# Kernel tuning notes

Measured on AMD Instinct MI355X. Metric: run time of the kernel, lower is better.

Reference implementation:

```python
import jax, jax.numpy as jnp
import numpy as np

N, E, B, NPG, LD, LT = 32768, 524288, 256, 128, 100, 1000

def conv1d(x, w, b):
    # x: [B, Cin, L], w: [Cout, Cin, K]
    y = jax.lax.conv_general_dilated(x, w, (1,), 'VALID', dimension_numbers=('NCH', 'OIH', 'NCH'))
    return y + b[None, :, None]

def conv_branch(x, w1, b1, w2, b2, w3, b3):
    x = jax.nn.relu(conv1d(x, w1, b1))
    x = jax.nn.relu(conv1d(x, w2, b2))
    x = jax.nn.relu(conv1d(x, w3, b3))
    return x.max(axis=2)  # global max pool over length

def gat(x, src, dst, ea, W, a_s, a_d, We, a_e, bias, heads, ch):
    # PyG GATConv with edge_dim, add_self_loops=True (fill_value='mean'), concat=True
    n = x.shape[0]
    loop = jnp.arange(n)
    src = jnp.concatenate([src, loop])
    dst = jnp.concatenate([dst, loop])
    ea = jnp.concatenate([ea, jnp.broadcast_to(ea.mean(0), (n, ea.shape[1]))], 0)
    h = (x @ W).reshape(n, heads, ch)                               # [N,H,C]
    a = (h * a_s).sum(-1)[src] + (h * a_d).sum(-1)[dst] \
        + ((ea @ We).reshape(-1, heads, ch) * a_e).sum(-1)          # [E+N,H]
    a = jax.nn.leaky_relu(a, 0.2)
    amax = jax.ops.segment_max(a, dst, num_segments=n)
    ex = jnp.exp(a - amax[dst])
    alpha = ex / (jax.ops.segment_sum(ex, dst, num_segments=n)[dst] + 1e-16)
    out = jax.ops.segment_sum(h[src] * alpha[..., None], dst, num_segments=n)
    return out.reshape(n, heads * ch) + bias

def reference(xd, xt, ax, ei, ea, batch, emb_xd, emb_xt, wd1, bd1, wd2, bd2, wd3, bd3, wt1, bt1, wt2, bt2, wt3, bt3, g1_w, g1_as, g1_ad, g1_we, g1_ae, g1_b, g2_w, g2_as, g2_ad, g2_we, g2_ae, g2_b, fc1_w, fc1_b, c1_w, c1_b, c2_w, c2_b, c3_w, c3_b, c4_w, c4_b):
    cd = conv_branch(emb_xd[xd].transpose(0, 2, 1), wd1, bd1, wd2, bd2, wd3, bd3)  # [B,96]
    ct = conv_branch(emb_xt[xt].transpose(0, 2, 1), wt1, bt1, wt2, bt2, wt3, bt3)  # [B,96]
    src, dst = ei[0], ei[1]
    g = jax.nn.elu(gat(ax, src, dst, ea, g1_w, g1_as, g1_ad, g1_we, g1_ae, g1_b, 5, 64))
    g = jax.nn.relu(gat(g, src, dst, ea, g2_w, g2_as, g2_ad, g2_we, g2_ae, g2_b, 1, 96))
    g = jax.ops.segment_max(g, batch, num_segments=B)               # global max pool per graph
    g = jax.nn.relu(g @ fc1_w + fc1_b)
    xc = jnp.concatenate([cd, ct, g], axis=1)                        # [B,288]
    h = jax.nn.relu(xc @ c1_w + c1_b)
    h = jax.nn.relu(h @ c2_w + c2_b)
    h = jax.nn.relu(h @ c3_w + c3_b)
    return h @ c4_w + c4_b                                           # [B,1]

def setup_inputs():
    ks = iter(jax.random.split(jax.random.key(0), 64))
    def nrm(*shape):
        return jax.random.normal(next(ks), shape, jnp.float32) * 0.05
    d = {}
    d['xd'] = jax.random.randint(next(ks), (B, LD), 0, 65, jnp.int32)
    d['xt'] = jax.random.randint(next(ks), (B, LT), 0, 26, jnp.int32)
    d['ax'] = jax.random.normal(next(ks), (N, 24), jnp.float32)
    gid = jax.random.randint(next(ks), (E,), 0, B)
    so = jax.random.randint(next(ks), (E,), 0, NPG)
    do = jax.random.randint(next(ks), (E,), 0, NPG)
    d['ei'] = jnp.stack([gid * NPG + so, gid * NPG + do]).astype(jnp.int32)
    d['ea'] = jax.random.normal(next(ks), (E, 5), jnp.float32)
    d['batch'] = jnp.repeat(jnp.arange(B, dtype=jnp.int32), NPG)
    d['emb_xd'] = nrm(65, 128); d['emb_xt'] = nrm(26, 128)
    d['wd1'] = nrm(32, 128, 4); d['bd1'] = nrm(32)
    d['wd2'] = nrm(64, 32, 4); d['bd2'] = nrm(64)
    d['wd3'] = nrm(96, 64, 4); d['bd3'] = nrm(96)
    d['wt1'] = nrm(32, 128, 8); d['bt1'] = nrm(32)
    d['wt2'] = nrm(64, 32, 8); d['bt2'] = nrm(64)
    d['wt3'] = nrm(96, 64, 8); d['bt3'] = nrm(96)
    d['g1_w'] = nrm(24, 320); d['g1_as'] = nrm(5, 64); d['g1_ad'] = nrm(5, 64)
    d['g1_we'] = nrm(5, 320); d['g1_ae'] = nrm(5, 64); d['g1_b'] = nrm(320)
    d['g2_w'] = nrm(320, 96); d['g2_as'] = nrm(1, 96); d['g2_ad'] = nrm(1, 96)
    d['g2_we'] = nrm(5, 96); d['g2_ae'] = nrm(1, 96); d['g2_b'] = nrm(96)
    d['fc1_w'] = nrm(96, 96); d['fc1_b'] = nrm(96)
    d['c1_w'] = nrm(288, 1024); d['c1_b'] = nrm(1024)
    d['c2_w'] = nrm(1024, 1024); d['c2_b'] = nrm(1024)
    d['c3_w'] = nrm(1024, 512); d['c3_b'] = nrm(512)
    d['c4_w'] = nrm(512, 1); d['c4_b'] = nrm(1)
    return d
```

## Files before the change

kernel.cpp:

```cpp
#include <hip/hip_runtime.h>

constexpr int NN = 32768;
constexpr int EE = 524288;
constexpr int NB = 256;
constexpr int EN = EE + NN;

typedef unsigned short u16;
typedef short bh8 __attribute__((ext_vector_type(8)));
typedef float f32x4 __attribute__((ext_vector_type(4)));

__device__ inline u16 f2b(float f) {
  unsigned u = __float_as_uint(f);
  return (u16)((u + 0x7fffu + ((u >> 16) & 1u)) >> 16);
}

constexpr size_t MB = 1ull << 20;
constexpr size_t OFF_A    = 0;
constexpr size_t OFF_B    = 48*MB;
constexpr size_t OFF_AC   = 100*MB;
constexpr size_t OFF_C    = 116*MB;
constexpr size_t OFF_CSRS = 130*MB;
constexpr size_t OFF_CSRE = 133*MB;
constexpr size_t OFF_ROWP = 136*MB;
constexpr size_t OFF_DEG  = 137*MB;
constexpr size_t OFF_CUR  = 138*MB;
constexpr size_t OFF_A2   = 139*MB;
constexpr size_t OFF_G2O  = 142*MB;
constexpr size_t OFF_AS1  = 155*MB;
constexpr size_t OFF_AD1  = 156*MB;
constexpr size_t OFF_AS2  = 157*MB;
constexpr size_t OFF_AD2  = 158*MB;
constexpr size_t OFF_CD   = 159*MB;
constexpr size_t OFF_CT   = 160*MB;
constexpr size_t OFF_POOL = 161*MB;
constexpr size_t OFF_GFC  = 162*MB;
constexpr size_t OFF_XC   = 163*MB;
constexpr size_t OFF_M1B  = 164*MB;
constexpr size_t OFF_M2B  = 165*MB;
constexpr size_t OFF_M3B  = 166*MB;
constexpr size_t OFF_FD   = 167*MB;
constexpr size_t OFF_FT   = 168*MB;
constexpr size_t OFF_WD2T = 169*MB;
constexpr size_t OFF_WD3T = 170*MB;
constexpr size_t OFF_WT2B = 171*MB;
constexpr size_t OFF_WT3B = 172*MB;
constexpr size_t OFF_W2GB = 174*MB;
constexpr size_t OFF_CB   = 173*MB;

__global__ void k_tables(const float* __restrict__ wd1, const float* __restrict__ emb_xd,
                         const float* __restrict__ wt1, const float* __restrict__ emb_xt,
                         const float* __restrict__ g1we, const float* __restrict__ g1ae,
                         const float* __restrict__ g2we, const float* __restrict__ g2ae,
                         float* __restrict__ Fd, float* __restrict__ Ft,
                         float* __restrict__ CB) {
  int t = blockIdx.x * 256 + threadIdx.x;
  const int NFd = 32*4*65, NFt = 32*8*26;
  if (t < NFd) {
    int v = t % 65; int ck = t / 65; int k = ck & 3; int co = ck >> 2;
    float s = 0.f;
    for (int ci = 0; ci < 128; ++ci)
      s = fmaf(wd1[(co*128 + ci)*4 + k], emb_xd[v*128 + ci], s);
    Fd[t] = s;
  } else if (t < NFd + NFt) {
    int u = t - NFd;
    int v = u % 26; int ck = u / 26; int k = ck & 7; int co = ck >> 3;
    float s = 0.f;
    for (int ci = 0; ci < 128; ++ci)
      s = fmaf(wt1[(co*128 + ci)*8 + k], emb_xt[v*128 + ci], s);
    Ft[(k*26 + v)*32 + co] = s;
  } else if (t < NFd + NFt + 25) {
    int u = t - NFd - NFt; int h = u % 5, j = u / 5;
    float s = 0.f;
    for (int c = 0; c < 64; ++c)
      s = fmaf(g1we[j*320 + h*64 + c], g1ae[h*64 + c], s);
    CB[j*5 + h] = s;
  } else if (t < NFd + NFt + 30) {
    int j = t - NFd - NFt - 25;
    float s = 0.f;
    for (int c = 0; c < 96; ++c)
      s = fmaf(g2we[j*96 + c], g2ae[c], s);
    CB[25 + j] = s;
  }
}

__global__ void k_wcvt(const float* __restrict__ w2, const float* __restrict__ w3,
                       const float* __restrict__ g2w,
                       u16* __restrict__ o2, u16* __restrict__ o3,
                       u16* __restrict__ og2) {
  int t = blockIdx.x*256 + threadIdx.x;
  if (t < 64*256) {
    int co = t >> 8, k = t & 255, kk = k >> 5, ci = k & 31;
    o2[t] = f2b(w2[(co*32 + ci)*8 + kk]);
  } else if (t < 64*256 + 96*512) {
    int u = t - 64*256;
    int co = u >> 9, k = u & 511, kk = k >> 6, ci = k & 63;
    o3[u] = f2b(w3[(co*64 + ci)*8 + kk]);
  } else if (t < 64*256 + 96*512 + 96*320) {
    int u = t - 64*256 - 96*512;
    int co = u / 320, k = u % 320;
    og2[u] = f2b(g2w[k*96 + co]);
  }
}

__global__ void k_easum(const float* __restrict__ ea, float* __restrict__ CB) {
  float acc[5] = {0,0,0,0,0};
  for (long e = blockIdx.x*256L + threadIdx.x; e < EE; e += 256L*gridDim.x) {
    #pragma unroll
    for (int j = 0; j < 5; ++j) acc[j] += ea[e*5 + j];
  }
  #pragma unroll
  for (int j = 0; j < 5; ++j)
    for (int off = 1; off < 64; off <<= 1) acc[j] += __shfl_xor(acc[j], off, 64);
  if ((threadIdx.x & 63) == 0) {
    #pragma unroll
    for (int j = 0; j < 5; ++j) atomicAdd(&CB[30 + j], acc[j]);
  }
}

__global__ void k_finalize(float* __restrict__ CB) {
  if (blockIdx.x == 0 && threadIdx.x == 0) {
    float em[5];
    for (int j = 0; j < 5; ++j) { em[j] = CB[30 + j] / (float)EE; CB[41 + j] = em[j]; }
    for (int h = 0; h < 5; ++h) {
      float s = 0.f;
      for (int j = 0; j < 5; ++j) s = fmaf(em[j], CB[j*5 + h], s);
      CB[35 + h] = s;
    }
    float s = 0.f;
    for (int j = 0; j < 5; ++j) s = fmaf(em[j], CB[25 + j], s);
    CB[40] = s;
  }
}

template<int K, int V, int COUT>
__global__ void k_conv1_lut(const int* __restrict__ idx, const float* __restrict__ F,
                            const float* __restrict__ bias, float* __restrict__ y,
                            int L, int Lout) {
  __shared__ float Fs[COUT*K*V];
  __shared__ float bs[COUT];
  int b = blockIdx.y;
  for (int i = threadIdx.x; i < COUT*K*V; i += blockDim.x) Fs[i] = F[i];
  for (int i = threadIdx.x; i < COUT; i += blockDim.x) bs[i] = bias[i];
  __syncthreads();
  int o = blockIdx.x * blockDim.x + threadIdx.x;
  if (o >= COUT * Lout) return;
  int co = o / Lout, l = o % Lout;
  const int* ib = idx + b*L + l;
  float acc = bs[co];
  #pragma unroll
  for (int k = 0; k < K; ++k) acc += Fs[(co*K + k)*V + ib[k]];
  y[(b*COUT + co)*Lout + l] = fmaxf(acc, 0.f);
}

__global__ __launch_bounds__(512) void k_conv1t(
    const int* __restrict__ idx, const float* __restrict__ Ftab,
    const float* __restrict__ bias, u16* __restrict__ y, int L, int Lout) {
  constexpr int K = 8, V = 26, CO = 32;
  __shared__ float Fs[K*V*CO];
  __shared__ float bs[CO];
  __shared__ int sq[16 + K];
  int b = blockIdx.y, l0 = blockIdx.x * 16;
  for (int i = threadIdx.x; i < K*V*CO; i += 512) Fs[i] = Ftab[i];
  if (threadIdx.x < CO) bs[threadIdx.x] = bias[threadIdx.x];
  if (threadIdx.x < 16 + K - 1) {
    int l = l0 + (int)threadIdx.x;
    sq[threadIdx.x] = (l < L) ? idx[b*L + l] : 0;
  }
  __syncthreads();
  int co = threadIdx.x & 31;
  int p = threadIdx.x >> 5;
  int l = l0 + p;
  if (l >= Lout) return;
  float acc = bs[co];
  #pragma unroll
  for (int k = 0; k < K; ++k) acc += Fs[(k*V + sq[p + k])*CO + co];
  y[((size_t)b*Lout + l)*CO + co] = f2b(fmaxf(acc, 0.f));
}

__global__ void k_wtrans(const float* __restrict__ w, float* __restrict__ wt,
                         int COUT, int CIN, int K) {
  int t = blockIdx.x*256 + threadIdx.x;
  if (t >= COUT*CIN*K) return;
  int k = t % K; int ci = (t / K) % CIN; int co = t / (K*CIN);
  wt[(ci*K + k)*COUT + co] = w[t];
}

template<int CIN, int K, int COUT, int G, int LG, bool POOL>
__global__ void k_conv(const float* __restrict__ x, const float* __restrict__ wt,
                       const float* __restrict__ bias, float* __restrict__ y,
                       int Lin, int Lout) {
  constexpr int LT = G * LG;
  __shared__ float xs[CIN][LT + K - 1];
  int b = blockIdx.y;
  int l0 = blockIdx.x * LT;
  const int nth = COUT * G;
  const float* xb = x + b*CIN*Lin;
  for (int i = threadIdx.x; i < CIN*(LT + K - 1); i += nth) {
    int ci = i / (LT + K - 1), dl = i % (LT + K - 1);
    int l = l0 + dl;
    xs[ci][dl] = (l < Lin) ? xb[ci*Lin + l] : 0.f;
  }
  __syncthreads();
  int co = threadIdx.x % COUT;
  int gg = threadIdx.x / COUT;
  float acc[LG];
  #pragma unroll
  for (int j = 0; j < LG; ++j) acc[j] = 0.f;
  for (int ci = 0; ci < CIN; ++ci) {
    float xr[LG + K - 1];
    #pragma unroll
    for (int t = 0; t < LG + K - 1; ++t) xr[t] = xs[ci][gg*LG + t];
    #pragma unroll
    for (int k = 0; k < K; ++k) {
      float wv = wt[(ci*K + k)*COUT + co];
      #pragma unroll
      for (int j = 0; j < LG; ++j) acc[j] = fmaf(wv, xr[j + k], acc[j]);
    }
  }
  float bv = bias[co];
  if (!POOL) {
    float* yb = y + (b*COUT + co)*Lout;
    #pragma unroll
    for (int j = 0; j < LG; ++j) {
      int l = l0 + gg*LG + j;
      if (l < Lout) yb[l] = fmaxf(acc[j] + bv, 0.f);
    }
  } else {
    float m = 0.f;
    #pragma unroll
    for (int j = 0; j < LG; ++j) {
      int l = l0 + gg*LG + j;
      if (l < Lout) m = fmaxf(m, fmaxf(acc[j] + bv, 0.f));
    }
    atomicMax((unsigned int*)&y[b*COUT + co], __float_as_uint(m));
  }
}

template<int CIN, int COUT, int NT2, bool POOL>
__global__ __launch_bounds__(512) void k_convmfma(
    const u16* __restrict__ xin, const u16* __restrict__ wtb,
    const float* __restrict__ bias, u16* __restrict__ yout,
    unsigned int* __restrict__ pool, int Lin, int Lout) {
  constexpr int KD = CIN*8;
  constexpr int NCH = KD/32;
  constexpr int MT = 256, ROWS = MT + 7;
  constexpr int XPAD = CIN + 8;
  constexpr int WPAD = KD + 8;
  __shared__ u16 xs[ROWS*XPAD];
  __shared__ u16 wsd[COUT*WPAD];
  int b = blockIdx.y;
  int l0 = blockIdx.x * MT;
  int tid = threadIdx.x;
  {
    const unsigned* wg = (const unsigned*)wtb;
    unsigned* wl = (unsigned*)wsd;
    constexpr int KD2 = KD/2, WP2 = WPAD/2;
    for (int i = tid; i < COUT*KD2; i += 512) {
      int co = i / KD2, c = i % KD2;
      wl[co*WP2 + c] = wg[i];
    }
  }
  {
    const unsigned* xg = (const unsigned*)(xin + (size_t)b*Lin*CIN);
    unsigned* xl = (unsigned*)xs;
    constexpr int C2 = CIN/2, XP2 = XPAD/2;
    for (int i = tid; i < ROWS*C2; i += 512) {
      int r = i / C2, c = i % C2;
      unsigned v = 0;
      if (l0 + r < Lin) v = xg[(size_t)l0*C2 + i];
      xl[r*XP2 + c] = v;
    }
  }
  __syncthreads();
  int lane = tid & 63;
  int w = tid >> 6;
  int mg = w & 3, ng = w >> 2;
  int l15 = lane & 15, l4 = lane >> 4;
  f32x4 acc[4][NT2];
  #pragma unroll
  for (int mi = 0; mi < 4; ++mi)
    #pragma unroll
    for (int nj = 0; nj < NT2; ++nj) acc[mi][nj] = (f32x4){0.f, 0.f, 0.f, 0.f};

  #pragma unroll
  for (int ch = 0; ch < NCH; ++ch) {
    const int kk = (ch*32) / CIN;
    const int cib = (ch*32) % CIN + l4*8;
    bh8 a[4], bb[NT2];
    #pragma unroll
    for (int mi = 0; mi < 4; ++mi) {
      int row = mg*64 + mi*16 + l15 + kk;
      a[mi] = *(const bh8*)&xs[row*XPAD + cib];
    }
    #pragma unroll
    for (int nj = 0; nj < NT2; ++nj) {
      int co = (ng*NT2 + nj)*16 + l15;
      bb[nj] = *(const bh8*)&wsd[co*WPAD + ch*32 + l4*8];
    }
    #pragma unroll
    for (int mi = 0; mi < 4; ++mi)
      #pragma unroll
      for (int nj = 0; nj < NT2; ++nj)
        acc[mi][nj] = __builtin_amdgcn_mfma_f32_16x16x32_bf16(a[mi], bb[nj], acc[mi][nj], 0, 0, 0);
  }

  if (!POOL) {
    #pragma unroll
    for (int nj = 0; nj < NT2; ++nj) {
      int co = (ng*NT2 + nj)*16 + l15;
      float bv = bias[co];
      #pragma unroll
      for (int mi = 0; mi < 4; ++mi)
        #pragma unroll
        for (int r = 0; r < 4; ++r) {
          int m = mg*64 + mi*16 + l4*4 + r;
          if (l0 + m < Lout)
            yout[((size_t)b*Lout + l0 + m)*COUT + co] = f2b(fmaxf(acc[mi][nj][r] + bv, 0.f));
        }
    }
  } else {
    #pragma unroll
    for (int nj = 0; nj < NT2; ++nj) {
      int co = (ng*NT2 + nj)*16 + l15;
      float bv = bias[co];
      float mx = 0.f;
      #pragma unroll
      for (int mi = 0; mi < 4; ++mi)
        #pragma unroll
        for (int r = 0; r < 4; ++r) {
          int m = mg*64 + mi*16 + l4*4 + r;
          if (l0 + m < Lout) mx = fmaxf(mx, fmaxf(acc[mi][nj][r] + bv, 0.f));
        }
      mx = fmaxf(mx, __shfl_xor(mx, 16, 64));
      mx = fmaxf(mx, __shfl_xor(mx, 32, 64));
      if (l4 == 0) atomicMax(&pool[b*COUT + co], __float_as_uint(mx));
    }
  }
}

__global__ __launch_bounds__(512) void k_h2mfma(
    const u16* __restrict__ g1ob, const u16* __restrict__ wb,
    float* __restrict__ h2) {
  constexpr int KD = 320, WPAD = 328, NCH = 10;
  __shared__ u16 wsd[96*WPAD];
  int tid = threadIdx.x;
  {
    const unsigned* wg = (const unsigned*)wb;
    unsigned* wl = (unsigned*)wsd;
    for (int i = tid; i < 96*(KD/2); i += 512) {
      int co = i / (KD/2), c = i % (KD/2);
      wl[co*(WPAD/2) + c] = wg[i];
    }
  }
  __syncthreads();
  int lane = tid & 63;
  int w = tid >> 6;
  int l15 = lane & 15, l4 = lane >> 4;
  long m0 = (long)blockIdx.x * 128;
  const u16* xr = g1ob + (m0 + w*16 + l15) * KD;
  f32x4 acc[6];
  #pragma unroll
  for (int nj = 0; nj < 6; ++nj) acc[nj] = (f32x4){0.f, 0.f, 0.f, 0.f};
  #pragma unroll
  for (int ch = 0; ch < NCH; ++ch) {
    bh8 a = *(const bh8*)&xr[ch*32 + l4*8];
    #pragma unroll
    for (int nj = 0; nj < 6; ++nj) {
      bh8 b = *(const bh8*)&wsd[(nj*16 + l15)*WPAD + ch*32 + l4*8];
      acc[nj] = __builtin_amdgcn_mfma_f32_16x16x32_bf16(a, b, acc[nj], 0, 0, 0);
    }
  }
  #pragma unroll
  for (int nj = 0; nj < 6; ++nj) {
    #pragma unroll
    for (int r = 0; r < 4; ++r) {
      long row = m0 + w*16 + l4*4 + r;
      h2[row*96 + nj*16 + l15] = acc[nj][r];
    }
  }
}

template<int BM, int BN, int BK, int TM, int TN, bool BIAS, bool RELU>
__global__ void k_gemm(const float* __restrict__ X, const float* __restrict__ W,
                       const float* __restrict__ bias, float* __restrict__ Y,
                       int K, int C) {
  constexpr int NTH = (BM/TM)*(BN/TN);
  static_assert(NTH == 256, "block must be 256 threads");
  __shared__ float xs[BK][BM + 1];
  __shared__ float wsm[BK][BN];
  const int m0 = blockIdx.y * BM;
  const int c0 = blockIdx.x * BN;
  const int tn = threadIdx.x % (BN/TN);
  const int tm = threadIdx.x / (BN/TN);
  float acc[TM][TN];
  #pragma unroll
  for (int i = 0; i < TM; ++i)
    #pragma unroll
    for (int j = 0; j < TN; ++j) acc[i][j] = 0.f;

  for (int k0 = 0; k0 < K; k0 += BK) {
    #pragma unroll
    for (int i = threadIdx.x; i < BM*BK; i += NTH) {
      int m = i / BK, k = i % BK;
      xs[k][m] = X[(long)(m0 + m)*K + k0 + k];
    }
    #pragma unroll
    for (int i = threadIdx.x; i < BK*BN; i += NTH) {
      int k = i / BN, c = i % BN;
      wsm[k][c] = W[(long)(k0 + k)*C + c0 + c];
    }
    __syncthreads();
    #pragma unroll
    for (int k = 0; k < BK; ++k) {
      float xv[TM], wv[TN];
      #pragma unroll
      for (int i = 0; i < TM; ++i) xv[i] = xs[k][tm*TM + i];
      #pragma unroll
      for (int j = 0; j < TN; ++j) wv[j] = wsm[k][tn*TN + j];
      #pragma unroll
      for (int i = 0; i < TM; ++i)
        #pragma unroll
        for (int j = 0; j < TN; ++j) acc[i][j] = fmaf(xv[i], wv[j], acc[i][j]);
    }
    __syncthreads();
  }
  #pragma unroll
  for (int i = 0; i < TM; ++i) {
    float* yr = Y + (long)(m0 + tm*TM + i)*C + c0 + tn*TN;
    #pragma unroll
    for (int j = 0; j < TN; ++j) {
      float v = acc[i][j];
      if (BIAS) v += bias[c0 + tn*TN + j];
      if (RELU) v = fmaxf(v, 0.f);
      yr[j] = v;
    }
  }
}

template<int BM, int BN, int BK, int TM, int TN>
__global__ void k_gemm_sk(const float* __restrict__ X, const float* __restrict__ W,
                          float* __restrict__ Y, int K, int C, int KS) {
  constexpr int NTH = (BM/TM)*(BN/TN);
  static_assert(NTH == 256, "block must be 256 threads");
  __shared__ float xs[BK][BM + 1];
  __shared__ float wsm[BK][BN];
  const int m0 = blockIdx.y * BM;
  const int c0 = blockIdx.x * BN;
  const int kbeg = blockIdx.z * KS;
  const int kend = min(K, kbeg + KS);
  const int tn = threadIdx.x % (BN/TN);
  const int tm = threadIdx.x / (BN/TN);
  float acc[TM][TN];
  #pragma unroll
  for (int i = 0; i < TM; ++i)
    #pragma unroll
    for (int j = 0; j < TN; ++j) acc[i][j] = 0.f;

  for (int k0 = kbeg; k0 < kend; k0 += BK) {
    #pragma unroll
    for (int i = threadIdx.x; i < BM*BK; i += NTH) {
      int m = i / BK, k = i % BK;
      xs[k][m] = X[(long)(m0 + m)*K + k0 + k];
    }
    #pragma unroll
    for (int i = threadIdx.x; i < BK*BN; i += NTH) {
      int k = i / BN, c = i % BN;
      wsm[k][c] = W[(long)(k0 + k)*C + c0 + c];
    }
    __syncthreads();
    #pragma unroll
    for (int k = 0; k < BK; ++k) {
      float xv[TM], wv[TN];
      #pragma unroll
      for (int i = 0; i < TM; ++i) xv[i] = xs[k][tm*TM + i];
      #pragma unroll
      for (int j = 0; j < TN; ++j) wv[j] = wsm[k][tn*TN + j];
      #pragma unroll
      for (int i = 0; i < TM; ++i)
        #pragma unroll
        for (int j = 0; j < TN; ++j) acc[i][j] = fmaf(xv[i], wv[j], acc[i][j]);
    }
    __syncthreads();
  }
  #pragma unroll
  for (int i = 0; i < TM; ++i) {
    float* yr = Y + (long)(m0 + tm*TM + i)*C + c0 + tn*TN;
    #pragma unroll
    for (int j = 0; j < TN; ++j) atomicAdd(&yr[j], acc[i][j]);
  }
}

__global__ void k_bias_relu(float* __restrict__ Y, const float* __restrict__ bias,
                            long total, int C, int relu) {
  long o = blockIdx.x*256L + threadIdx.x;
  if (o >= total) return;
  int c = (int)(o % C);
  float v = Y[o] + bias[c];
  if (relu) v = fmaxf(v, 0.f);
  Y[o] = v;
}

__global__ void k_attn_nodeterms(const float* __restrict__ h, const float* __restrict__ a_s,
                                 const float* __restrict__ a_d, float* __restrict__ as_o,
                                 float* __restrict__ ad_o, int H, int CH) {
  long t = blockIdx.x*256L + threadIdx.x;
  if (t >= (long)NN * H) return;
  int n = (int)(t / H), hh = (int)(t % H);
  const float* hr = h + ((long)n*H + hh)*CH;
  float s1 = 0.f, s2 = 0.f;
  for (int c = 0; c < CH; ++c) {
    float v = hr[c];
    s1 = fmaf(v, a_s[hh*CH + c], s1);
    s2 = fmaf(v, a_d[hh*CH + c], s2);
  }
  as_o[t] = s1; ad_o[t] = s2;
}

template<int H>
__global__ void k_edge_attn(const int* __restrict__ ei, const float* __restrict__ ea,
                            const float* __restrict__ asb, const float* __restrict__ adb,
                            const float* __restrict__ M, const float* __restrict__ aeself,
                            float* __restrict__ a_out) {
  long e = blockIdx.x*256L + threadIdx.x;
  if (e >= (long)EN) return;
  int s, d;
  float av[H];
  if (e < EE) {
    s = ei[e]; d = ei[EE + e];
    float er[5];
    #pragma unroll
    for (int j = 0; j < 5; ++j) er[j] = ea[e*5 + j];
    #pragma unroll
    for (int h = 0; h < H; ++h) {
      float t = 0.f;
      #pragma unroll
      for (int j = 0; j < 5; ++j) t = fmaf(er[j], M[j*H + h], t);
      av[h] = t;
    }
  } else {
    s = d = (int)(e - EE);
    #pragma unroll
    for (int h = 0; h < H; ++h) av[h] = aeself[h];
  }
  #pragma unroll
  for (int h = 0; h < H; ++h) {
    float v = asb[s*H + h] + adb[d*H + h] + av[h];
    a_out[e*H + h] = (v > 0.f) ? v : 0.2f * v;
  }
}

template<int H>
__global__ void k_acsr(const int* __restrict__ csr_eid, const float* __restrict__ a,
                       float* __restrict__ ac) {
  long p = blockIdx.x*256L + threadIdx.x;
  if (p >= (long)EN) return;
  long e = csr_eid[p];
  #pragma unroll
  for (int h = 0; h < H; ++h) ac[p*H + h] = a[e*H + h];
}

__global__ void k_deg(const int* __restrict__ ei, int* __restrict__ deg) {
  long e = blockIdx.x*256L + threadIdx.x;
  if (e >= (long)EN) return;
  int d = (e < EE) ? ei[EE + e] : (int)(e - EE);
  atomicAdd(&deg[d], 1);
}

__global__ void k_scan(const int* __restrict__ deg, int* __restrict__ rowptr,
                       int* __restrict__ cursor) {
  __shared__ int ps[256];
  int tid = threadIdx.x;
  int base = tid * 128;
  int s = 0;
  for (int i = 0; i < 128; ++i) s += deg[base + i];
  ps[tid] = s;
  __syncthreads();
  for (int off = 1; off < 256; off <<= 1) {
    int v = (tid >= off) ? ps[tid - off] : 0;
    __syncthreads();
    ps[tid] += v;
    __syncthreads();
  }
  int run = ps[tid] - s;
  for (int i = 0; i < 128; ++i) {
    rowptr[base + i] = run;
    cursor[base + i] = run;
    run += deg[base + i];
  }
  if (tid == 255) rowptr[NN] = run;
}

__global__ void k_scatter(const int* __restrict__ ei, int* __restrict__ cursor,
                          int* __restrict__ csr_src, int* __restrict__ csr_eid) {
  long e = blockIdx.x*256L + threadIdx.x;
  if (e >= (long)EN) return;
  int s, d;
  if (e < EE) { s = ei[e]; d = ei[EE + e]; }
  else        { s = d = (int)(e - EE); }
  int p = atomicAdd(&cursor[d], 1);
  csr_src[p] = s;
  csr_eid[p] = (int)e;
}

template<int H, int CH, int ACT, bool OBF16>
__global__ void k_gat_aggr(const int* __restrict__ rowptr, const int* __restrict__ csr_src,
                           const float* __restrict__ ac,
                           const float* __restrict__ hfeat, const float* __restrict__ bias,
                           void* __restrict__ outv) {
  int bid = blockIdx.x;
  int x = bid & 7;
  int r = bid >> 3;
  int s = r & 31;
  int c = r >> 5;
  int g = c*8 + x;
  int wid = g*128 + s*4 + (int)(threadIdx.x >> 6);
  int lane = threadIdx.x & 63;
  int row0 = rowptr[wid], row1 = rowptr[wid + 1];
  constexpr int F = H * CH;
  constexpr int NJ = (F + 63) / 64;
  float amax[H], asum[H], rinv[H];
  #pragma unroll
  for (int h = 0; h < H; ++h) amax[h] = -1e30f;
  for (int p = row0 + lane; p < row1; p += 64) {
    #pragma unroll
    for (int h = 0; h < H; ++h) amax[h] = fmaxf(amax[h], ac[(long)p*H + h]);
  }
  #pragma unroll
  for (int h = 0; h < H; ++h)
    for (int off = 1; off < 64; off <<= 1) amax[h] = fmaxf(amax[h], __shfl_xor(amax[h], off, 64));
  #pragma unroll
  for (int h = 0; h < H; ++h) asum[h] = 0.f;
  for (int p = row0 + lane; p < row1; p += 64) {
    #pragma unroll
    for (int h = 0; h < H; ++h) asum[h] += __expf(ac[(long)p*H + h] - amax[h]);
  }
  #pragma unroll
  for (int h = 0; h < H; ++h) {
    for (int off = 1; off < 64; off <<= 1) asum[h] += __shfl_xor(asum[h], off, 64);
    rinv[h] = 1.f / (asum[h] + 1e-16f);
  }
  float acc[NJ];
  #pragma unroll
  for (int j = 0; j < NJ; ++j) acc[j] = 0.f;
  for (int p = row0; p < row1; ++p) {
    int src = csr_src[p];
    const float* hr = hfeat + (long)src * F;
    #pragma unroll
    for (int j = 0; j < NJ; ++j) {
      int idx = j*64 + lane;
      if ((F % 64 == 0) || idx < F) {
        int h = idx / CH;
        float al = __expf(ac[(long)p*H + h] - amax[h]) * rinv[h];
        acc[j] = fmaf(al, hr[idx], acc[j]);
      }
    }
  }
  #pragma unroll
  for (int j = 0; j < NJ; ++j) {
    int idx = j*64 + lane;
    if ((F % 64 == 0) || idx < F) {
      float v = acc[j] + bias[idx];
      if (ACT == 0) v = (v > 0.f) ? v : expm1f(v);
      else          v = fmaxf(v, 0.f);
      if (OBF16) ((u16*)outv)[(long)wid * F + idx] = f2b(v);
      else       ((float*)outv)[(long)wid * F + idx] = v;
    }
  }
}

__global__ void k_pool(const float* __restrict__ g2o, const int* __restrict__ batch,
                       unsigned int* __restrict__ pooled) {
  long o = blockIdx.x*256L + threadIdx.x;
  if (o >= (long)NN * 96) return;
  int n = (int)(o / 96), c = (int)(o % 96);
  atomicMax(&pooled[batch[n]*96 + c], __float_as_uint(g2o[o]));
}

__global__ void k_concat(const float* __restrict__ cd, const float* __restrict__ ct,
                         const float* __restrict__ gfc, float* __restrict__ xc) {
  int t = blockIdx.x*256 + threadIdx.x;
  if (t >= NB*288) return;
  int b = t / 288, c = t % 288;
  float v = (c < 96) ? cd[b*96 + c] : (c < 192) ? ct[b*96 + (c-96)] : gfc[b*96 + (c-192)];
  xc[t] = v;
}

__global__ void k_final(const float* __restrict__ x, const float* __restrict__ w,
                        const float* __restrict__ b, float* __restrict__ out) {
  int wid = (int)((blockIdx.x*256L + threadIdx.x) >> 6);
  int lane = threadIdx.x & 63;
  if (wid >= NB) return;
  const float* xr = x + (long)wid*512;
  float s = 0.f;
  for (int k = lane; k < 512; k += 64) s = fmaf(xr[k], w[k], s);
  for (int off = 1; off < 64; off <<= 1) s += __shfl_xor(s, off, 64);
  if (lane == 0) out[wid] = s + b[0];
}

extern "C" void kernel_launch(void* const* d_in, const int* in_sizes, int n_in,
                              void* d_out, int out_size, void* d_ws, size_t ws_size,
                              hipStream_t stream) {
  const int*   xd     = (const int*)  d_in[0];
  const int*   xt     = (const int*)  d_in[1];
  const float* ax     = (const float*)d_in[2];
  const int*   ei     = (const int*)  d_in[3];
  const float* ea     = (const float*)d_in[4];
  const int*   batch  = (const int*)  d_in[5];
  const float* emb_xd = (const float*)d_in[6];
  const float* emb_xt = (const float*)d_in[7];
  const float* wd1 = (const float*)d_in[8];  const float* bd1 = (const float*)d_in[9];
  const float* wd2 = (const float*)d_in[10]; const float* bd2 = (const float*)d_in[11];
  const float* wd3 = (const float*)d_in[12]; const float* bd3 = (const float*)d_in[13];
  const float* wt1 = (const float*)d_in[14]; const float* bt1 = (const float*)d_in[15];
  const float* wt2 = (const float*)d_in[16]; const float* bt2 = (const float*)d_in[17];
  const float* wt3 = (const float*)d_in[18]; const float* bt3 = (const float*)d_in[19];
  const float* g1_w  = (const float*)d_in[20]; const float* g1_as = (const float*)d_in[21];
  const float* g1_ad = (const float*)d_in[22]; const float* g1_we = (const float*)d_in[23];
  const float* g1_ae = (const float*)d_in[24]; const float* g1_b  = (const float*)d_in[25];
  const float* g2_w  = (const float*)d_in[26]; const float* g2_as = (const float*)d_in[27];
  const float* g2_ad = (const float*)d_in[28]; const float* g2_we = (const float*)d_in[29];
  const float* g2_ae = (const float*)d_in[30]; const float* g2_b  = (const float*)d_in[31];
  const float* fc1_w = (const float*)d_in[32]; const float* fc1_b = (const float*)d_in[33];
  const float* c1_w = (const float*)d_in[34]; const float* c1_b = (const float*)d_in[35];
  const float* c2_w = (const float*)d_in[36]; const float* c2_b = (const float*)d_in[37];
  const float* c3_w = (const float*)d_in[38]; const float* c3_b = (const float*)d_in[39];
  const float* c4_w = (const float*)d_in[40]; const float* c4_b = (const float*)d_in[41];
  float* out = (float*)d_out;

  char* ws = (char*)d_ws;
  auto F = [&](size_t off) { return (float*)(ws + off); };
  auto I = [&](size_t off) { return (int*)(ws + off); };
  auto U = [&](size_t off) { return (unsigned int*)(ws + off); };
  auto H = [&](size_t off) { return (u16*)(ws + off); };

  hipMemsetAsync(ws + OFF_CB,   0, 64*sizeof(float), stream);
  hipMemsetAsync(ws + OFF_DEG,  0, NN*sizeof(int),   stream);
  hipMemsetAsync(ws + OFF_CD,   0, NB*96*sizeof(float), stream);
  hipMemsetAsync(ws + OFF_CT,   0, NB*96*sizeof(float), stream);
  hipMemsetAsync(ws + OFF_POOL, 0, NB*96*sizeof(float), stream);
  hipMemsetAsync(ws + OFF_GFC,  0, NB*96*sizeof(float),   stream);
  hipMemsetAsync(ws + OFF_M1B,  0, NB*1024*sizeof(float), stream);
  hipMemsetAsync(ws + OFF_M2B,  0, NB*1024*sizeof(float), stream);
  hipMemsetAsync(ws + OFF_M3B,  0, NB*512*sizeof(float),  stream);

  k_tables<<<(8320 + 6656 + 30 + 255)/256, 256, 0, stream>>>(
      wd1, emb_xd, wt1, emb_xt, g1_we, g1_ae, g2_we, g2_ae,
      F(OFF_FD), F(OFF_FT), F(OFF_CB));
  k_wcvt<<<(64*256 + 96*512 + 96*320 + 255)/256, 256, 0, stream>>>(
      wt2, wt3, g2_w, H(OFF_WT2B), H(OFF_WT3B), H(OFF_W2GB));
  k_easum<<<256, 256, 0, stream>>>(ea, F(OFF_CB));
  k_finalize<<<1, 64, 0, stream>>>(F(OFF_CB));

  k_wtrans<<<(8192 + 255)/256, 256, 0, stream>>>(wd2, F(OFF_WD2T), 64, 32, 4);
  k_wtrans<<<(24576 + 255)/256, 256, 0, stream>>>(wd3, F(OFF_WD3T), 96, 64, 4);

  k_conv1_lut<4,65,32><<<dim3((32*97 + 255)/256, NB), 256, 0, stream>>>(
      xd, F(OFF_FD), bd1, F(OFF_A), 100, 97);
  k_conv<32,4,64,4,16,false><<<dim3((94 + 63)/64, NB), 256, 0, stream>>>(
      F(OFF_A), F(OFF_WD2T), bd2, F(OFF_B), 97, 94);
  k_conv<64,4,96,2,16,true><<<dim3((91 + 31)/32, NB), 192, 0, stream>>>(
      F(OFF_B), F(OFF_WD3T), bd3, F(OFF_CD), 94, 91);

  k_conv1t<<<dim3((993 + 15)/16, NB), 512, 0, stream>>>(
      xt, F(OFF_FT), bt1, H(OFF_A), 1000, 993);
  k_convmfma<32,64,2,false><<<dim3(4, NB), 512, 0, stream>>>(
      H(OFF_A), H(OFF_WT2B), bt2, H(OFF_B), nullptr, 993, 986);
  k_convmfma<64,96,3,true><<<dim3(4, NB), 512, 0, stream>>>(
      H(OFF_B), H(OFF_WT3B), bt3, nullptr, U(OFF_CT), 986, 979);

  k_deg<<<(EN + 255)/256, 256, 0, stream>>>(ei, I(OFF_DEG));
  k_scan<<<1, 256, 0, stream>>>(I(OFF_DEG), I(OFF_ROWP), I(OFF_CUR));
  k_scatter<<<(EN + 255)/256, 256, 0, stream>>>(ei, I(OFF_CUR), I(OFF_CSRS), I(OFF_CSRE));

  k_gemm<64,64,24,4,4,false,false><<<dim3(320/64, NN/64), 256, 0, stream>>>(
      ax, g1_w, nullptr, F(OFF_A), 24, 320);
  k_attn_nodeterms<<<(NN*5 + 255)/256, 256, 0, stream>>>(
      F(OFF_A), g1_as, g1_ad, F(OFF_AS1), F(OFF_AD1), 5, 64);
  k_edge_attn<5><<<(EN + 255)/256, 256, 0, stream>>>(
      ei, ea, F(OFF_AS1), F(OFF_AD1), F(OFF_CB), F(OFF_CB) + 35, F(OFF_C));
  k_acsr<5><<<(EN + 255)/256, 256, 0, stream>>>(
      I(OFF_CSRE), F(OFF_C), F(OFF_AC));
  k_gat_aggr<5,64,0,true><<<NN/4, 256, 0, stream>>>(
      I(OFF_ROWP), I(OFF_CSRS), F(OFF_AC), F(OFF_A), g1_b, (void*)H(OFF_B));

  k_h2mfma<<<NN/128, 512, 0, stream>>>(H(OFF_B), H(OFF_W2GB), F(OFF_C));
  k_attn_nodeterms<<<(NN + 255)/256, 256, 0, stream>>>(
      F(OFF_C), g2_as, g2_ad, F(OFF_AS2), F(OFF_AD2), 1, 96);
  k_edge_attn<1><<<(EN + 255)/256, 256, 0, stream>>>(
      ei, ea, F(OFF_AS2), F(OFF_AD2), F(OFF_CB) + 25, F(OFF_CB) + 40, F(OFF_A2));
  k_acsr<1><<<(EN + 255)/256, 256, 0, stream>>>(
      I(OFF_CSRE), F(OFF_A2), F(OFF_AC));
  k_gat_aggr<1,96,1,false><<<NN/4, 256, 0, stream>>>(
      I(OFF_ROWP), I(OFF_CSRS), F(OFF_AC), F(OFF_C), g2_b, (void*)F(OFF_G2O));

  k_pool<<<(int)(((long)NN*96 + 255)/256), 256, 0, stream>>>(
      F(OFF_G2O), batch, U(OFF_POOL));
  k_gemm_sk<64,32,32,4,2><<<dim3(96/32, NB/64, 3), 256, 0, stream>>>(
      F(OFF_POOL), fc1_w, F(OFF_GFC), 96, 96, 32);
  k_bias_relu<<<(NB*96 + 255)/256, 256, 0, stream>>>(
      F(OFF_GFC), fc1_b, (long)NB*96, 96, 1);

  k_concat<<<(NB*288 + 255)/256, 256, 0, stream>>>(
      F(OFF_CD), F(OFF_CT), F(OFF_GFC), F(OFF_XC));

  k_gemm_sk<64,64,32,4,4><<<dim3(1024/64, NB/64, 3), 256, 0, stream>>>(
      F(OFF_XC), c1_w, F(OFF_M1B), 288, 1024, 96);
  k_bias_relu<<<(NB*1024 + 255)/256, 256, 0, stream>>>(
      F(OFF_M1B), c1_b, (long)NB*1024, 1024, 1);

  k_gemm_sk<64,64,32,4,4><<<dim3(1024/64, NB/64, 8), 256, 0, stream>>>(
      F(OFF_M1B), c2_w, F(OFF_M2B), 1024, 1024, 128);
  k_bias_relu<<<(NB*1024 + 255)/256, 256, 0, stream>>>(
      F(OFF_M2B), c2_b, (long)NB*1024, 1024, 1);

  k_gemm_sk<64,64,32,4,4><<<dim3(512/64, NB/64, 8), 256, 0, stream>>>(
      F(OFF_M2B), c3_w, F(OFF_M3B), 1024, 512, 128);
  k_bias_relu<<<(NB*512 + 255)/256, 256, 0, stream>>>(
      F(OFF_M3B), c3_b, (long)NB*512, 512, 1);

  k_final<<<(NB*64 + 255)/256, 256, 0, stream>>>(F(OFF_M3B), c4_w, c4_b, out);
}
```

Measured before the change: 882.4 us.

## Move drug conv branch to bf16 MFMA and split GAT softmax into separate kernels

The drug-sequence conv branch now uses the same LUT-based first layer and bf16 MFMA conv kernels as the target branch, replacing the fp32 scalar conv kernels and the weight transpose kernels. Separately, the GAT softmax max/sum pass moves out of the aggregation kernel into a per-node stats kernel, followed by an edge-parallel kernel that writes normalized alpha in place. For that, the CSR build now also records each edge's destination. The aggregation kernel then only does the weighted sum, at the cost of two extra launches per layer and extra passes over the edge array.

```diff
diff --git a/kernel.cpp b/kernel.cpp
--- a/kernel.cpp
+++ b/kernel.cpp
@@ -18,6 +18,7 @@
 constexpr size_t OFF_A    = 0;
 constexpr size_t OFF_B    = 48*MB;
 constexpr size_t OFF_AC   = 100*MB;
+constexpr size_t OFF_CSRD = 112*MB;
 constexpr size_t OFF_C    = 116*MB;
 constexpr size_t OFF_CSRS = 130*MB;
 constexpr size_t OFF_CSRE = 133*MB;
@@ -40,8 +41,8 @@
 constexpr size_t OFF_M3B  = 166*MB;
 constexpr size_t OFF_FD   = 167*MB;
 constexpr size_t OFF_FT   = 168*MB;
-constexpr size_t OFF_WD2T = 169*MB;
-constexpr size_t OFF_WD3T = 170*MB;
+constexpr size_t OFF_WD2B = 169*MB;
+constexpr size_t OFF_WD3B = 170*MB;
 constexpr size_t OFF_WT2B = 171*MB;
 constexpr size_t OFF_WT3B = 172*MB;
 constexpr size_t OFF_W2GB = 174*MB;
@@ -60,7 +61,7 @@
     float s = 0.f;
     for (int ci = 0; ci < 128; ++ci)
       s = fmaf(wd1[(co*128 + ci)*4 + k], emb_xd[v*128 + ci], s);
-    Fd[t] = s;
+    Fd[(k*65 + v)*32 + co] = s;
   } else if (t < NFd + NFt) {
     int u = t - NFd;
     int v = u % 26; int ck = u / 26; int k = ck & 7; int co = ck >> 3;
@@ -83,22 +84,28 @@
   }
 }
 
-__global__ void k_wcvt(const float* __restrict__ w2, const float* __restrict__ w3,
+__global__ void k_wcvt(const float* __restrict__ wd2, const float* __restrict__ wd3,
+                       const float* __restrict__ wt2, const float* __restrict__ wt3,
                        const float* __restrict__ g2w,
-                       u16* __restrict__ o2, u16* __restrict__ o3,
+                       u16* __restrict__ od2, u16* __restrict__ od3,
+                       u16* __restrict__ ot2, u16* __restrict__ ot3,
                        u16* __restrict__ og2) {
   int t = blockIdx.x*256 + threadIdx.x;
-  if (t < 64*256) {
+  if (t < 8192) {
+    int co = t >> 7, k = t & 127, kk = k >> 5, ci = k & 31;
+    od2[t] = f2b(wd2[(co*32 + ci)*4 + kk]);
+  } else if ((t -= 8192) < 24576) {
+    int co = t >> 8, k = t & 255, kk = k >> 6, ci = k & 63;
+    od3[t] = f2b(wd3[(co*64 + ci)*4 + kk]);
+  } else if ((t -= 24576) < 16384) {
     int co = t >> 8, k = t & 255, kk = k >> 5, ci = k & 31;
-    o2[t] = f2b(w2[(co*32 + ci)*8 + kk]);
-  } else if (t < 64*256 + 96*512) {
-    int u = t - 64*256;
-    int co = u >> 9, k = u & 511, kk = k >> 6, ci = k & 63;
-    o3[u] = f2b(w3[(co*64 + ci)*8 + kk]);
-  } else if (t < 64*256 + 96*512 + 96*320) {
-    int u = t - 64*256 - 96*512;
-    int co = u / 320, k = u % 320;
-    og2[u] = f2b(g2w[k*96 + co]);
+    ot2[t] = f2b(wt2[(co*32 + ci)*8 + kk]);
+  } else if ((t -= 16384) < 49152) {
+    int co = t >> 9, k = t & 511, kk = k >> 6, ci = k & 63;
+    ot3[t] = f2b(wt3[(co*64 + ci)*8 + kk]);
+  } else if ((t -= 49152) < 30720) {
+    int co = t / 320, k = t % 320;
+    og2[t] = f2b(g2w[k*96 + co]);
   }
 }
 
@@ -132,30 +139,11 @@
   }
 }
 
-template<int K, int V, int COUT>
-__global__ void k_conv1_lut(const int* __restrict__ idx, const float* __restrict__ F,
-                            const float* __restrict__ bias, float* __restrict__ y,
-                            int L, int Lout) {
-  __shared__ float Fs[COUT*K*V];
-  __shared__ float bs[COUT];
-  int b = blockIdx.y;
-  for (int i = threadIdx.x; i < COUT*K*V; i += blockDim.x) Fs[i] = F[i];
-  for (int i = threadIdx.x; i < COUT; i += blockDim.x) bs[i] = bias[i];
-  __syncthreads();
-  int o = blockIdx.x * blockDim.x + threadIdx.x;
-  if (o >= COUT * Lout) return;
-  int co = o / Lout, l = o % Lout;
-  const int* ib = idx + b*L + l;
-  float acc = bs[co];
-  #pragma unroll
-  for (int k = 0; k < K; ++k) acc += Fs[(co*K + k)*V + ib[k]];
-  y[(b*COUT + co)*Lout + l] = fmaxf(acc, 0.f);
-}
-
+template<int K, int V>
 __global__ __launch_bounds__(512) void k_conv1t(
     const int* __restrict__ idx, const float* __restrict__ Ftab,
     const float* __restrict__ bias, u16* __restrict__ y, int L, int Lout) {
-  constexpr int K = 8, V = 26, CO = 32;
+  constexpr int CO = 32;
   __shared__ float Fs[K*V*CO];
   __shared__ float bs[CO];
   __shared__ int sq[16 + K];
@@ -177,73 +165,14 @@
   y[((size_t)b*Lout + l)*CO + co] = f2b(fmaxf(acc, 0.f));
 }
 
-__global__ void k_wtrans(const float* __restrict__ w, float* __restrict__ wt,
-                         int COUT, int CIN, int K) {
-  int t = blockIdx.x*256 + threadIdx.x;
-  if (t >= COUT*CIN*K) return;
-  int k = t % K; int ci = (t / K) % CIN; int co = t / (K*CIN);
-  wt[(ci*K + k)*COUT + co] = w[t];
-}
-
-template<int CIN, int K, int COUT, int G, int LG, bool POOL>
-__global__ void k_conv(const float* __restrict__ x, const float* __restrict__ wt,
-                       const float* __restrict__ bias, float* __restrict__ y,
-                       int Lin, int Lout) {
-  constexpr int LT = G * LG;
-  __shared__ float xs[CIN][LT + K - 1];
-  int b = blockIdx.y;
-  int l0 = blockIdx.x * LT;
-  const int nth = COUT * G;
-  const float* xb = x + b*CIN*Lin;
-  for (int i = threadIdx.x; i < CIN*(LT + K - 1); i += nth) {
-    int ci = i / (LT + K - 1), dl = i % (LT + K - 1);
-    int l = l0 + dl;
-    xs[ci][dl] = (l < Lin) ? xb[ci*Lin + l] : 0.f;
-  }
-  __syncthreads();
-  int co = threadIdx.x % COUT;
-  int gg = threadIdx.x / COUT;
-  float acc[LG];
-  #pragma unroll
-  for (int j = 0; j < LG; ++j) acc[j] = 0.f;
-  for (int ci = 0; ci < CIN; ++ci) {
-    float xr[LG + K - 1];
-    #pragma unroll
-    for (int t = 0; t < LG + K - 1; ++t) xr[t] = xs[ci][gg*LG + t];
-    #pragma unroll
-    for (int k = 0; k < K; ++k) {
-      float wv = wt[(ci*K + k)*COUT + co];
-      #pragma unroll
-      for (int j = 0; j < LG; ++j) acc[j] = fmaf(wv, xr[j + k], acc[j]);
-    }
-  }
-  float bv = bias[co];
-  if (!POOL) {
-    float* yb = y + (b*COUT + co)*Lout;
-    #pragma unroll
-    for (int j = 0; j < LG; ++j) {
-      int l = l0 + gg*LG + j;
-      if (l < Lout) yb[l] = fmaxf(acc[j] + bv, 0.f);
-    }
-  } else {
-    float m = 0.f;
-    #pragma unroll
-    for (int j = 0; j < LG; ++j) {
-      int l = l0 + gg*LG + j;
-      if (l < Lout) m = fmaxf(m, fmaxf(acc[j] + bv, 0.f));
-    }
-    atomicMax((unsigned int*)&y[b*COUT + co], __float_as_uint(m));
-  }
-}
-
-template<int CIN, int COUT, int NT2, bool POOL>
+template<int CIN, int KK, int COUT, int NT2, bool POOL>
 __global__ __launch_bounds__(512) void k_convmfma(
     const u16* __restrict__ xin, const u16* __restrict__ wtb,
     const float* __restrict__ bias, u16* __restrict__ yout,
     unsigned int* __restrict__ pool, int Lin, int Lout) {
-  constexpr int KD = CIN*8;
+  constexpr int KD = CIN*KK;
   constexpr int NCH = KD/32;
-  constexpr int MT = 256, ROWS = MT + 7;
+  constexpr int MT = 256, ROWS = MT + KK - 1;
   constexpr int XPAD = CIN + 8;
   constexpr int WPAD = KD + 8;
   __shared__ u16 xs[ROWS*XPAD];
@@ -559,6 +488,52 @@
   for (int h = 0; h < H; ++h) ac[p*H + h] = a[e*H + h];
 }
 
+template<int H>
+__global__ void k_stats(const int* __restrict__ rowptr, const float* __restrict__ ac,
+                        float* __restrict__ amaxo, float* __restrict__ rinvo) {
+  int wid = (int)((blockIdx.x*256L + threadIdx.x) >> 6);
+  int lane = threadIdx.x & 63;
+  if (wid >= NN) return;
+  int row0 = rowptr[wid], row1 = rowptr[wid + 1];
+  float amax[H], asum[H];
+  #pragma unroll
+  for (int h = 0; h < H; ++h) amax[h] = -1e30f;
+  for (int p = row0 + lane; p < row1; p += 64) {
+    #pragma unroll
+    for (int h = 0; h < H; ++h) amax[h] = fmaxf(amax[h], ac[(long)p*H + h]);
+  }
+  #pragma unroll
+  for (int h = 0; h < H; ++h)
+    for (int off = 1; off < 64; off <<= 1) amax[h] = fmaxf(amax[h], __shfl_xor(amax[h], off, 64));
+  #pragma unroll
+  for (int h = 0; h < H; ++h) asum[h] = 0.f;
+  for (int p = row0 + lane; p < row1; p += 64) {
+    #pragma unroll
+    for (int h = 0; h < H; ++h) asum[h] += __expf(ac[(long)p*H + h] - amax[h]);
+  }
+  #pragma unroll
+  for (int h = 0; h < H; ++h)
+    for (int off = 1; off < 64; off <<= 1) asum[h] += __shfl_xor(asum[h], off, 64);
+  if (lane == 0) {
+    #pragma unroll
+    for (int h = 0; h < H; ++h) {
+      amaxo[(long)wid*H + h] = amax[h];
+      rinvo[(long)wid*H + h] = 1.f / (asum[h] + 1e-16f);
+    }
+  }
+}
+
+template<int H>
+__global__ void k_alpha(const int* __restrict__ csr_dst, const float* __restrict__ amaxb,
+                        const float* __restrict__ rinvb, float* __restrict__ ac) {
+  long p = blockIdx.x*256L + threadIdx.x;
+  if (p >= (long)EN) return;
+  int d = csr_dst[p];
+  #pragma unroll
+  for (int h = 0; h < H; ++h)
+    ac[p*H + h] = __expf(ac[p*H + h] - amaxb[(long)d*H + h]) * rinvb[(long)d*H + h];
+}
+
 __global__ void k_deg(const int* __restrict__ ei, int* __restrict__ deg) {
   long e = blockIdx.x*256L + threadIdx.x;
   if (e >= (long)EN) return;
@@ -591,7 +566,8 @@
 }
 
 __global__ void k_scatter(const int* __restrict__ ei, int* __restrict__ cursor,
-                          int* __restrict__ csr_src, int* __restrict__ csr_eid) {
+                          int* __restrict__ csr_src, int* __restrict__ csr_eid,
+                          int* __restrict__ csr_dst) {
   long e = blockIdx.x*256L + threadIdx.x;
   if (e >= (long)EN) return;
   int s, d;
@@ -600,6 +576,7 @@
   int p = atomicAdd(&cursor[d], 1);
   csr_src[p] = s;
   csr_eid[p] = (int)e;
+  csr_dst[p] = d;
 }
 
 template<int H, int CH, int ACT, bool OBF16>
@@ -618,27 +595,6 @@
   int row0 = rowptr[wid], row1 = rowptr[wid + 1];
   constexpr int F = H * CH;
   constexpr int NJ = (F + 63) / 64;
-  float amax[H], asum[H], rinv[H];
-  #pragma unroll
-  for (int h = 0; h < H; ++h) amax[h] = -1e30f;
-  for (int p = row0 + lane; p < row1; p += 64) {
-    #pragma unroll
-    for (int h = 0; h < H; ++h) amax[h] = fmaxf(amax[h], ac[(long)p*H + h]);
-  }
-  #pragma unroll
-  for (int h = 0; h < H; ++h)
-    for (int off = 1; off < 64; off <<= 1) amax[h] = fmaxf(amax[h], __shfl_xor(amax[h], off, 64));
-  #pragma unroll
-  for (int h = 0; h < H; ++h) asum[h] = 0.f;
-  for (int p = row0 + lane; p < row1; p += 64) {
-    #pragma unroll
-    for (int h = 0; h < H; ++h) asum[h] += __expf(ac[(long)p*H + h] - amax[h]);
-  }
-  #pragma unroll
-  for (int h = 0; h < H; ++h) {
-    for (int off = 1; off < 64; off <<= 1) asum[h] += __shfl_xor(asum[h], off, 64);
-    rinv[h] = 1.f / (asum[h] + 1e-16f);
-  }
   float acc[NJ];
   #pragma unroll
   for (int j = 0; j < NJ; ++j) acc[j] = 0.f;
@@ -650,8 +606,7 @@
       int idx = j*64 + lane;
       if ((F % 64 == 0) || idx < F) {
         int h = idx / CH;
-        float al = __expf(ac[(long)p*H + h] - amax[h]) * rinv[h];
-        acc[j] = fmaf(al, hr[idx], acc[j]);
+        acc[j] = fmaf(ac[(long)p*H + h], hr[idx], acc[j]);
       }
     }
   }
@@ -746,31 +701,30 @@
   k_tables<<<(8320 + 6656 + 30 + 255)/256, 256, 0, stream>>>(
       wd1, emb_xd, wt1, emb_xt, g1_we, g1_ae, g2_we, g2_ae,
       F(OFF_FD), F(OFF_FT), F(OFF_CB));
-  k_wcvt<<<(64*256 + 96*512 + 96*320 + 255)/256, 256, 0, stream>>>(
-      wt2, wt3, g2_w, H(OFF_WT2B), H(OFF_WT3B), H(OFF_W2GB));
+  k_wcvt<<<(8192 + 24576 + 16384 + 49152 + 30720 + 255)/256, 256, 0, stream>>>(
+      wd2, wd3, wt2, wt3, g2_w,
+      H(OFF_WD2B), H(OFF_WD3B), H(OFF_WT2B), H(OFF_WT3B), H(OFF_W2GB));
   k_easum<<<256, 256, 0, stream>>>(ea, F(OFF_CB));
   k_finalize<<<1, 64, 0, stream>>>(F(OFF_CB));
 
-  k_wtrans<<<(8192 + 255)/256, 256, 0, stream>>>(wd2, F(OFF_WD2T), 64, 32, 4);
-  k_wtrans<<<(24576 + 255)/256, 256, 0, stream>>>(wd3, F(OFF_WD3T), 96, 64, 4);
-
-  k_conv1_lut<4,65,32><<<dim3((32*97 + 255)/256, NB), 256, 0, stream>>>(
-      xd, F(OFF_FD), bd1, F(OFF_A), 100, 97);
-  k_conv<32,4,64,4,16,false><<<dim3((94 + 63)/64, NB), 256, 0, stream>>>(
-      F(OFF_A), F(OFF_WD2T), bd2, F(OFF_B), 97, 94);
-  k_conv<64,4,96,2,16,true><<<dim3((91 + 31)/32, NB), 192, 0, stream>>>(
-      F(OFF_B), F(OFF_WD3T), bd3, F(OFF_CD), 94, 91);
-
-  k_conv1t<<<dim3((993 + 15)/16, NB), 512, 0, stream>>>(
+  k_conv1t<4,65><<<dim3((97 + 15)/16, NB), 512, 0, stream>>>(
+      xd, F(OFF_FD), bd1, H(OFF_A), 100, 97);
+  k_convmfma<32,4,64,2,false><<<dim3(1, NB), 512, 0, stream>>>(
+      H(OFF_A), H(OFF_WD2B), bd2, H(OFF_B), nullptr, 97, 94);
+  k_convmfma<64,4,96,3,true><<<dim3(1, NB), 512, 0, stream>>>(
+      H(OFF_B), H(OFF_WD3B), bd3, nullptr, U(OFF_CD), 94, 91);
+
+  k_conv1t<8,26><<<dim3((993 + 15)/16, NB), 512, 0, stream>>>(
       xt, F(OFF_FT), bt1, H(OFF_A), 1000, 993);
-  k_convmfma<32,64,2,false><<<dim3(4, NB), 512, 0, stream>>>(
+  k_convmfma<32,8,64,2,false><<<dim3(4, NB), 512, 0, stream>>>(
       H(OFF_A), H(OFF_WT2B), bt2, H(OFF_B), nullptr, 993, 986);
-  k_convmfma<64,96,3,true><<<dim3(4, NB), 512, 0, stream>>>(
+  k_convmfma<64,8,96,3,true><<<dim3(4, NB), 512, 0, stream>>>(
       H(OFF_B), H(OFF_WT3B), bt3, nullptr, U(OFF_CT), 986, 979);
 
   k_deg<<<(EN + 255)/256, 256, 0, stream>>>(ei, I(OFF_DEG));
   k_scan<<<1, 256, 0, stream>>>(I(OFF_DEG), I(OFF_ROWP), I(OFF_CUR));
-  k_scatter<<<(EN + 255)/256, 256, 0, stream>>>(ei, I(OFF_CUR), I(OFF_CSRS), I(OFF_CSRE));
+  k_scatter<<<(EN + 255)/256, 256, 0, stream>>>(
+      ei, I(OFF_CUR), I(OFF_CSRS), I(OFF_CSRE), I(OFF_CSRD));
 
   k_gemm<64,64,24,4,4,false,false><<<dim3(320/64, NN/64), 256, 0, stream>>>(
       ax, g1_w, nullptr, F(OFF_A), 24, 320);
@@ -780,6 +734,10 @@
       ei, ea, F(OFF_AS1), F(OFF_AD1), F(OFF_CB), F(OFF_CB) + 35, F(OFF_C));
   k_acsr<5><<<(EN + 255)/256, 256, 0, stream>>>(
       I(OFF_CSRE), F(OFF_C), F(OFF_AC));
+  k_stats<5><<<NN/4, 256, 0, stream>>>(
+      I(OFF_ROWP), F(OFF_AC), F(OFF_AS1), F(OFF_AD1));
+  k_alpha<5><<<(EN + 255)/256, 256, 0, stream>>>(
+      I(OFF_CSRD), F(OFF_AS1), F(OFF_AD1), F(OFF_AC));
   k_gat_aggr<5,64,0,true><<<NN/4, 256, 0, stream>>>(
       I(OFF_ROWP), I(OFF_CSRS), F(OFF_AC), F(OFF_A), g1_b, (void*)H(OFF_B));
 
@@ -790,6 +748,10 @@
       ei, ea, F(OFF_AS2), F(OFF_AD2), F(OFF_CB) + 25, F(OFF_CB) + 40, F(OFF_A2));
   k_acsr<1><<<(EN + 255)/256, 256, 0, stream>>>(
       I(OFF_CSRE), F(OFF_A2), F(OFF_AC));
+  k_stats<1><<<NN/4, 256, 0, stream>>>(
+      I(OFF_ROWP), F(OFF_AC), F(OFF_AS2), F(OFF_AD2));
+  k_alpha<1><<<(EN + 255)/256, 256, 0, stream>>>(
+      I(OFF_CSRD), F(OFF_AS2), F(OFF_AD2), F(OFF_AC));
   k_gat_aggr<1,96,1,false><<<NN/4, 256, 0, stream>>>(
       I(OFF_ROWP), I(OFF_CSRS), F(OFF_AC), F(OFF_C), g2_b, (void*)F(OFF_G2O));
 
```

Result: no change. 876.7 us (-0.6%).
